# Kernel optimization log

Measured on AMD Instinct MI355X. Metric: run time of the kernel, lower is better.

The kernel has to match this reference:

```python
import jax, jax.numpy as jnp
import numpy as np


def _segment_softmax(x, seg, num_segments):
    # x: (E, C), seg: (E,) int. Numerically stable per-segment softmax along dim 0.
    m = jax.ops.segment_max(x, seg, num_segments=num_segments)  # (S, C)
    # Guard empty segments (-inf) so gather stays finite for used rows.
    e = jnp.exp(x - m[seg])                                     # (E, C)
    s = jax.ops.segment_sum(e, seg, num_segments=num_segments)  # (S, C)
    return e / s[seg]


def setup_inputs() -> dict:
    key = jax.random.key(0)
    k1, k2, k3, k4 = jax.random.split(key, 4)
    E, C, S = 16777216, 2, 4096
    return {
        "xab": jax.random.normal(k1, (E, C), dtype=jnp.float32),
        "xba": jax.random.normal(k2, (E, C), dtype=jnp.float32),
        "src_id": jax.random.randint(k3, (E,), 0, S, dtype=jnp.int64),
        "tar_id": jax.random.randint(k4, (E,), 0, S, dtype=jnp.int64),
        "num_segments": S,
    }


def reference(xab, xba, src_id, tar_id, num_segments):
    zab = _segment_softmax(xab, src_id, num_segments)  # softmax over src groups
    zba = _segment_softmax(xba, tar_id, num_segments)  # softmax over tar groups
    return (zab * zba, zab, zba)
```

## Files before the change

kernel.cpp:

```cpp
#include <hip/hip_runtime.h>

#define NSEG 4096
#define QSCALE 131072.0f
#define QINV   (1.0f / 131072.0f)

typedef unsigned long long u64;
typedef unsigned int u32;
typedef float f32x4 __attribute__((ext_vector_type(4)));
typedef float f32x2 __attribute__((ext_vector_type(2)));

__global__ __launch_bounds__(1024) void dsp_reduce_x(
    const f32x4* __restrict__ xab4, const f32x4* __restrict__ xba4,
    const int2* __restrict__ src2, const int2* __restrict__ tar2,
    float* __restrict__ partials,
    int rounds, int rs)
{
    __shared__ u64 ls[2 * NSEG];
    for (int i = threadIdx.x; i < 2 * NSEG; i += 1024) ls[i] = 0ull;
    __syncthreads();

    const int base = blockIdx.x * 1024 + threadIdx.x;
    int u = base + (rounds - 1) * rs;

    f32x4 a = xab4[u], b = xba4[u];
    int2 s = src2[u], t = tar2[u];

    for (int r = rounds - 1; r >= 0; --r) {
        int un = u - rs;
        f32x4 an, bn; int2 sn, tn;
        if (r > 0) { an = xab4[un]; bn = xba4[un]; sn = src2[un]; tn = tar2[un]; }

        u32 a0 = __float2uint_rn(__expf(a.x) * QSCALE);
        u32 a1 = __float2uint_rn(__expf(a.y) * QSCALE);
        u32 a2 = __float2uint_rn(__expf(a.z) * QSCALE);
        u32 a3 = __float2uint_rn(__expf(a.w) * QSCALE);
        atomicAdd(&ls[s.x], (u64)a0 | ((u64)a1 << 32));
        atomicAdd(&ls[s.y], (u64)a2 | ((u64)a3 << 32));

        u32 b0 = __float2uint_rn(__expf(b.x) * QSCALE);
        u32 b1 = __float2uint_rn(__expf(b.y) * QSCALE);
        u32 b2 = __float2uint_rn(__expf(b.z) * QSCALE);
        u32 b3 = __float2uint_rn(__expf(b.w) * QSCALE);
        atomicAdd(&ls[NSEG + t.x], (u64)b0 | ((u64)b1 << 32));
        atomicAdd(&ls[NSEG + t.y], (u64)b2 | ((u64)b3 << 32));

        u = un; a = an; b = bn; s = sn; t = tn;
    }
    __syncthreads();

    f32x2* dst = (f32x2*)(partials + (size_t)blockIdx.x * (4 * NSEG));
    for (int i = threadIdx.x; i < 2 * NSEG; i += 1024) {
        u64 v = ls[i];
        f32x2 w = { (float)(u32)v * QINV, (float)(u32)(v >> 32) * QINV };
        __builtin_nontemporal_store(w, &dst[i]);
    }
}

__global__ __launch_bounds__(1024) void dsp_reduce_g(
    const f32x4* __restrict__ xab4, const f32x4* __restrict__ xba4,
    const int2* __restrict__ src2, const int2* __restrict__ tar2,
    float* __restrict__ partials, int Eh)
{
    __shared__ u64 ls[2 * NSEG];
    for (int i = threadIdx.x; i < 2 * NSEG; i += 1024) ls[i] = 0ull;
    __syncthreads();

    const int stride = gridDim.x * 1024;
    for (int u = blockIdx.x * 1024 + threadIdx.x; u < Eh; u += stride) {
        f32x4 a = xab4[u]; f32x4 b = xba4[u];
        int2 s = src2[u]; int2 t = tar2[u];
        u32 a0 = __float2uint_rn(__expf(a.x) * QSCALE);
        u32 a1 = __float2uint_rn(__expf(a.y) * QSCALE);
        u32 a2 = __float2uint_rn(__expf(a.z) * QSCALE);
        u32 a3 = __float2uint_rn(__expf(a.w) * QSCALE);
        atomicAdd(&ls[s.x], (u64)a0 | ((u64)a1 << 32));
        atomicAdd(&ls[s.y], (u64)a2 | ((u64)a3 << 32));
        u32 b0 = __float2uint_rn(__expf(b.x) * QSCALE);
        u32 b1 = __float2uint_rn(__expf(b.y) * QSCALE);
        u32 b2 = __float2uint_rn(__expf(b.z) * QSCALE);
        u32 b3 = __float2uint_rn(__expf(b.w) * QSCALE);
        atomicAdd(&ls[NSEG + t.x], (u64)b0 | ((u64)b1 << 32));
        atomicAdd(&ls[NSEG + t.y], (u64)b2 | ((u64)b3 << 32));
    }
    __syncthreads();

    f32x2* dst = (f32x2*)(partials + (size_t)blockIdx.x * (4 * NSEG));
    for (int i = threadIdx.x; i < 2 * NSEG; i += 1024) {
        u64 v = ls[i];
        f32x2 w = { (float)(u32)v * QINV, (float)(u32)(v >> 32) * QINV };
        __builtin_nontemporal_store(w, &dst[i]);
    }
}

__global__ __launch_bounds__(256) void dsp_sum(
    const f32x4* __restrict__ partials, f32x4* __restrict__ rcp_out, int nb)
{
    int i = blockIdx.x * blockDim.x + threadIdx.x;
    f32x4 acc = {0.f, 0.f, 0.f, 0.f};
    for (int p = 0; p < nb; ++p) {
        f32x4 v = __builtin_nontemporal_load(&partials[(size_t)p * NSEG + i]);
        acc += v;
    }
    f32x4 r;
    r.x = (acc.x > 0.f) ? 1.f / acc.x : 0.f;
    r.y = (acc.y > 0.f) ? 1.f / acc.y : 0.f;
    r.z = (acc.z > 0.f) ? 1.f / acc.z : 0.f;
    r.w = (acc.w > 0.f) ? 1.f / acc.w : 0.f;
    rcp_out[i] = r;
}

__global__ __launch_bounds__(1024) void dsp_norm_x(
    const f32x4* __restrict__ xab4, const f32x4* __restrict__ xba4,
    const int2* __restrict__ src2, const int2* __restrict__ tar2,
    const f32x4* __restrict__ rcp_tab,
    f32x4* __restrict__ out, int rounds, int rs, int Eh)
{
    __shared__ float ls[4 * NSEG];
    for (int i = threadIdx.x; i < NSEG; i += 1024)
        ((f32x4*)ls)[i] = rcp_tab[i];
    __syncthreads();

    const int base = blockIdx.x * 1024 + threadIdx.x;
    int u = base;

    f32x4 a = xab4[u], b = xba4[u];
    int2 s = src2[u], t = tar2[u];

    for (int r = 0; r < rounds; ++r) {
        int un = u + rs;
        f32x4 an, bn; int2 sn, tn;
        if (r + 1 < rounds) { an = xab4[un]; bn = xba4[un]; sn = src2[un]; tn = tar2[un]; }

        f32x2 ra0 = *(const f32x2*)&ls[2 * s.x];
        f32x2 ra1 = *(const f32x2*)&ls[2 * s.y];
        f32x2 rb0 = *(const f32x2*)&ls[2 * NSEG + 2 * t.x];
        f32x2 rb1 = *(const f32x2*)&ls[2 * NSEG + 2 * t.y];

        f32x4 zab = { __expf(a.x) * ra0.x, __expf(a.y) * ra0.y,
                      __expf(a.z) * ra1.x, __expf(a.w) * ra1.y };
        f32x4 zba = { __expf(b.x) * rb0.x, __expf(b.y) * rb0.y,
                      __expf(b.z) * rb1.x, __expf(b.w) * rb1.y };
        f32x4 prod = zab * zba;

        __builtin_nontemporal_store(prod, &out[u]);
        __builtin_nontemporal_store(zab,  &out[Eh + u]);
        __builtin_nontemporal_store(zba,  &out[2 * Eh + u]);

        u = un; a = an; b = bn; s = sn; t = tn;
    }
}

__global__ __launch_bounds__(1024) void dsp_norm_g(
    const f32x4* __restrict__ xab4, const f32x4* __restrict__ xba4,
    const int2* __restrict__ src2, const int2* __restrict__ tar2,
    const f32x4* __restrict__ rcp_tab,
    f32x4* __restrict__ out, int Eh)
{
    __shared__ float ls[4 * NSEG];
    for (int i = threadIdx.x; i < NSEG; i += 1024)
        ((f32x4*)ls)[i] = rcp_tab[i];
    __syncthreads();

    const int stride = gridDim.x * 1024;
    for (int u = blockIdx.x * 1024 + threadIdx.x; u < Eh; u += stride) {
        f32x4 a = xab4[u]; f32x4 b = xba4[u];
        int2 s = src2[u]; int2 t = tar2[u];
        f32x2 ra0 = *(const f32x2*)&ls[2 * s.x];
        f32x2 ra1 = *(const f32x2*)&ls[2 * s.y];
        f32x2 rb0 = *(const f32x2*)&ls[2 * NSEG + 2 * t.x];
        f32x2 rb1 = *(const f32x2*)&ls[2 * NSEG + 2 * t.y];
        f32x4 zab = { __expf(a.x) * ra0.x, __expf(a.y) * ra0.y,
                      __expf(a.z) * ra1.x, __expf(a.w) * ra1.y };
        f32x4 zba = { __expf(b.x) * rb0.x, __expf(b.y) * rb0.y,
                      __expf(b.z) * rb1.x, __expf(b.w) * rb1.y };
        f32x4 prod = zab * zba;
        __builtin_nontemporal_store(prod, &out[u]);
        __builtin_nontemporal_store(zab,  &out[Eh + u]);
        __builtin_nontemporal_store(zba,  &out[2 * Eh + u]);
    }
}

extern "C" void kernel_launch(void* const* d_in, const int* in_sizes, int n_in,
                              void* d_out, int out_size, void* d_ws, size_t ws_size,
                              hipStream_t stream)
{
    const int E  = in_sizes[0] / 2;
    const int Eh = E / 2;
    const f32x4* xab4 = (const f32x4*)d_in[0];
    const f32x4* xba4 = (const f32x4*)d_in[1];
    const int2*  src2 = (const int2*)d_in[2];
    const int2*  tar2 = (const int2*)d_in[3];

    const int NB = 512;
    const int RS = NB * 1024;
    float* rcp_tab  = (float*)d_ws;
    float* partials = (float*)((char*)d_ws + 65536);
    size_t need = 65536 + (size_t)NB * 65536;
    const bool exact = (ws_size >= need) && (Eh % RS == 0) && (Eh / RS >= 1);

    if (exact) {
        const int rounds = Eh / RS;
        dsp_reduce_x<<<NB, 1024, 0, stream>>>(xab4, xba4, src2, tar2,
                                              partials, rounds, RS);
        dsp_sum<<<NSEG / 256, 256, 0, stream>>>((const f32x4*)partials,
                                                (f32x4*)rcp_tab, NB);
        dsp_norm_x<<<NB, 1024, 0, stream>>>(xab4, xba4, src2, tar2,
                                            (const f32x4*)rcp_tab,
                                            (f32x4*)d_out, rounds, RS, Eh);
    } else {
        dsp_reduce_g<<<NB, 1024, 0, stream>>>(xab4, xba4, src2, tar2,
                                              partials, Eh);
        dsp_sum<<<NSEG / 256, 256, 0, stream>>>((const f32x4*)partials,
                                                (f32x4*)rcp_tab, NB);
        dsp_norm_g<<<NB, 1024, 0, stream>>>(xab4, xba4, src2, tar2,
                                            (const f32x4*)rcp_tab,
                                            (f32x4*)d_out, Eh);
    }
}
```

Measured before the change: 429.1 us.

## Fuse reduce, sum and normalize into one cooperative kernel with grid syncs

Replaces the three-launch pipeline with a single cooperative kernel that accumulates per-block segment sums, grid-syncs, reduces partials across blocks with warp shuffles, grid-syncs again, and then normalizes. The normalize pass walks rounds in reverse so the most recently read data may still be in cache, and the partials stores become normal instead of nontemporal so they stay cached for the cross-block sum. This removes launch gaps and gives some L2/MALL reuse, at the cost of grid-sync overhead and losing the explicit software prefetch in the loops. It depends on occupancy of at least 2 blocks per CU so that all 512 blocks are co-resident.

```diff
diff --git a/kernel.cpp b/kernel.cpp
--- a/kernel.cpp
+++ b/kernel.cpp
@@ -1,34 +1,40 @@
 #include <hip/hip_runtime.h>
+#include <hip/hip_cooperative_groups.h>
+
+namespace cg = cooperative_groups;
 
 #define NSEG 4096
 #define QSCALE 131072.0f
 #define QINV   (1.0f / 131072.0f)
+#define NB 512
 
 typedef unsigned long long u64;
 typedef unsigned int u32;
 typedef float f32x4 __attribute__((ext_vector_type(4)));
 typedef float f32x2 __attribute__((ext_vector_type(2)));
 
-__global__ __launch_bounds__(1024) void dsp_reduce_x(
+__global__ __launch_bounds__(1024, 8) void dsp_fused(
     const f32x4* __restrict__ xab4, const f32x4* __restrict__ xba4,
     const int2* __restrict__ src2, const int2* __restrict__ tar2,
     float* __restrict__ partials,
-    int rounds, int rs)
+    float* __restrict__ rcp_tab,
+    f32x4* __restrict__ out,
+    int rounds, int rs, int Eh)
 {
     __shared__ u64 ls[2 * NSEG];
-    for (int i = threadIdx.x; i < 2 * NSEG; i += 1024) ls[i] = 0ull;
-    __syncthreads();
-
-    const int base = blockIdx.x * 1024 + threadIdx.x;
-    int u = base + (rounds - 1) * rs;
-
-    f32x4 a = xab4[u], b = xba4[u];
-    int2 s = src2[u], t = tar2[u];
-
-    for (int r = rounds - 1; r >= 0; --r) {
-        int un = u - rs;
-        f32x4 an, bn; int2 sn, tn;
-        if (r > 0) { an = xab4[un]; bn = xba4[un]; sn = src2[un]; tn = tar2[un]; }
+    const int tid = threadIdx.x;
+    const int bid = blockIdx.x;
+    const int base = bid * 1024 + tid;
+
+    for (int i = tid; i < 2 * NSEG; i += 1024) ls[i] = 0ull;
+    __syncthreads();
+
+    for (int r = 0; r < rounds; ++r) {
+        int u = base + r * rs;
+        f32x4 a = xab4[u];
+        f32x4 b = xba4[u];
+        int2 s = src2[u];
+        int2 t = tar2[u];
 
         u32 a0 = __float2uint_rn(__expf(a.x) * QSCALE);
         u32 a1 = __float2uint_rn(__expf(a.y) * QSCALE);
@@ -43,16 +49,61 @@
         u32 b3 = __float2uint_rn(__expf(b.w) * QSCALE);
         atomicAdd(&ls[NSEG + t.x], (u64)b0 | ((u64)b1 << 32));
         atomicAdd(&ls[NSEG + t.y], (u64)b2 | ((u64)b3 << 32));
-
-        u = un; a = an; b = bn; s = sn; t = tn;
-    }
-    __syncthreads();
-
-    f32x2* dst = (f32x2*)(partials + (size_t)blockIdx.x * (4 * NSEG));
-    for (int i = threadIdx.x; i < 2 * NSEG; i += 1024) {
-        u64 v = ls[i];
-        f32x2 w = { (float)(u32)v * QINV, (float)(u32)(v >> 32) * QINV };
-        __builtin_nontemporal_store(w, &dst[i]);
+    }
+    __syncthreads();
+
+    {
+        f32x2* dst = (f32x2*)(partials + (size_t)bid * (4 * NSEG));
+        for (int i = tid; i < 2 * NSEG; i += 1024) {
+            u64 v = ls[i];
+            f32x2 w = { (float)(u32)v * QINV, (float)(u32)(v >> 32) * QINV };
+            dst[i] = w;
+        }
+    }
+    __threadfence();
+    cg::this_grid().sync();
+
+    {
+        int cl = tid >> 5;
+        int k  = tid & 31;
+        int col = bid * 32 + cl;
+        float acc = 0.f;
+        for (int p = k; p < NB; p += 32)
+            acc += partials[(size_t)p * (4 * NSEG) + col];
+        for (int off = 16; off; off >>= 1)
+            acc += __shfl_down(acc, off, 32);
+        if (k == 0)
+            rcp_tab[col] = (acc > 0.f) ? 1.f / acc : 0.f;
+    }
+    __threadfence();
+    cg::this_grid().sync();
+
+    float* lf = (float*)ls;
+    for (int i = tid; i < NSEG; i += 1024)
+        ((f32x4*)lf)[i] = ((const f32x4*)rcp_tab)[i];
+    __syncthreads();
+
+    for (int r = rounds - 1; r >= 0; --r) {
+        int u = base + r * rs;
+        f32x4 a = xab4[u];
+        f32x4 b = xba4[u];
+        int2 s = src2[u];
+        int2 t = tar2[u];
+
+        f32x2 ra0 = *(const f32x2*)&lf[2 * s.x];
+        f32x2 ra1 = *(const f32x2*)&lf[2 * s.y];
+        f32x2 rb0 = *(const f32x2*)&lf[2 * NSEG + 2 * t.x];
+        f32x2 rb1 = *(const f32x2*)&lf[2 * NSEG + 2 * t.y];
+
+        f32x4 zab = { __expf(a.x) * ra0.x, __expf(a.y) * ra0.y,
+                      __expf(a.z) * ra1.x, __expf(a.w) * ra1.y };
+        f32x4 zba = { __expf(b.x) * rb0.x, __expf(b.y) * rb0.y,
+                      __expf(b.z) * rb1.x, __expf(b.w) * rb1.y };
+        f32x4 prod = zab * zba;
+
+        __builtin_nontemporal_store(prod, &out[u]);
+        __builtin_nontemporal_store(zab,  &out[Eh + u]);
+        __builtin_nontemporal_store(zba,  &out[2 * Eh + u]);
     }
 }
 
@@ -88,7 +139,7 @@
     for (int i = threadIdx.x; i < 2 * NSEG; i += 1024) {
         u64 v = ls[i];
         f32x2 w = { (float)(u32)v * QINV, (float)(u32)(v >> 32) * QINV };
-        __builtin_nontemporal_store(w, &dst[i]);
+        dst[i] = w;
     }
 }
 
@@ -97,57 +148,14 @@
 {
     int i = blockIdx.x * blockDim.x + threadIdx.x;
     f32x4 acc = {0.f, 0.f, 0.f, 0.f};
-    for (int p = 0; p < nb; ++p) {
-        f32x4 v = __builtin_nontemporal_load(&partials[(size_t)p * NSEG + i]);
-        acc += v;
-    }
+    for (int p = 0; p < nb; ++p)
+        acc += partials[(size_t)p * NSEG + i];
     f32x4 r;
     r.x = (acc.x > 0.f) ? 1.f / acc.x : 0.f;
     r.y = (acc.y > 0.f) ? 1.f / acc.y : 0.f;
     r.z = (acc.z > 0.f) ? 1.f / acc.z : 0.f;
     r.w = (acc.w > 0.f) ? 1.f / acc.w : 0.f;
     rcp_out[i] = r;
-}
-
-__global__ __launch_bounds__(1024) void dsp_norm_x(
-    const f32x4* __restrict__ xab4, const f32x4* __restrict__ xba4,
-    const int2* __restrict__ src2, const int2* __restrict__ tar2,
-    const f32x4* __restrict__ rcp_tab,
-    f32x4* __restrict__ out, int rounds, int rs, int Eh)
-{
-    __shared__ float ls[4 * NSEG];
-    for (int i = threadIdx.x; i < NSEG; i += 1024)
-        ((f32x4*)ls)[i] = rcp_tab[i];
-    __syncthreads();
-
-    const int base = blockIdx.x * 1024 + threadIdx.x;
-    int u = base;
-
-    f32x4 a = xab4[u], b = xba4[u];
-    int2 s = src2[u], t = tar2[u];
-
-    for (int r = 0; r < rounds; ++r) {
-        int un = u + rs;
-        f32x4 an, bn; int2 sn, tn;
-        if (r + 1 < rounds) { an = xab4[un]; bn = xba4[un]; sn = src2[un]; tn = tar2[un]; }
-
-        f32x2 ra0 = *(const f32x2*)&ls[2 * s.x];
-        f32x2 ra1 = *(const f32x2*)&ls[2 * s.y];
-        f32x2 rb0 = *(const f32x2*)&ls[2 * NSEG + 2 * t.x];
-        f32x2 rb1 = *(const f32x2*)&ls[2 * NSEG + 2 * t.y];
-
-        f32x4 zab = { __expf(a.x) * ra0.x, __expf(a.y) * ra0.y,
-                      __expf(a.z) * ra1.x, __expf(a.w) * ra1.y };
-        f32x4 zba = { __expf(b.x) * rb0.x, __expf(b.y) * rb0.y,
-                      __expf(b.z) * rb1.x, __expf(b.w) * rb1.y };
-        f32x4 prod = zab * zba;
-
-        __builtin_nontemporal_store(prod, &out[u]);
-        __builtin_nontemporal_store(zab,  &out[Eh + u]);
-        __builtin_nontemporal_store(zba,  &out[2 * Eh + u]);
-
-        u = un; a = an; b = bn; s = sn; t = tn;
-    }
 }
 
 __global__ __launch_bounds__(1024) void dsp_norm_g(
@@ -191,22 +199,26 @@
     const int2*  src2 = (const int2*)d_in[2];
     const int2*  tar2 = (const int2*)d_in[3];
 
-    const int NB = 512;
     const int RS = NB * 1024;
     float* rcp_tab  = (float*)d_ws;
     float* partials = (float*)((char*)d_ws + 65536);
     size_t need = 65536 + (size_t)NB * 65536;
-    const bool exact = (ws_size >= need) && (Eh % RS == 0) && (Eh / RS >= 1);
-
-    if (exact) {
-        const int rounds = Eh / RS;
-        dsp_reduce_x<<<NB, 1024, 0, stream>>>(xab4, xba4, src2, tar2,
-                                              partials, rounds, RS);
-        dsp_sum<<<NSEG / 256, 256, 0, stream>>>((const f32x4*)partials,
-                                                (f32x4*)rcp_tab, NB);
-        dsp_norm_x<<<NB, 1024, 0, stream>>>(xab4, xba4, src2, tar2,
-                                            (const f32x4*)rcp_tab,
-                                            (f32x4*)d_out, rounds, RS, Eh);
+
+    int rounds = Eh / RS;
+    bool exact = (ws_size >= need) && (Eh % RS == 0) && (rounds >= 1);
+
+    int occ = 0;
+    (void)hipOccupancyMaxActiveBlocksPerMultiprocessor(&occ, dsp_fused, 1024, 0);
+
+    if (exact && occ >= 2) {
+        f32x4* outv = (f32x4*)d_out;
+        void* args[] = { (void*)&xab4, (void*)&xba4, (void*)&src2, (void*)&tar2,
+                         (void*)&partials, (void*)&rcp_tab, (void*)&outv,
+                         (void*)&rounds, (void*)&(int&)RS, (void*)&(int&)Eh };
+        int rs_v = RS, eh_v = Eh;
+        args[7] = (void*)&rounds; args[8] = (void*)&rs_v; args[9] = (void*)&eh_v;
+        (void)hipLaunchCooperativeKernel((void*)dsp_fused, dim3(NB), dim3(1024),
+                                         args, 0, stream);
     } else {
         dsp_reduce_g<<<NB, 1024, 0, stream>>>(xab4, xba4, src2, tar2,
                                               partials, Eh);
```

Result: faster. 356.9 us (-16.8%).

## Batch loads four-deep in reduce, prefetch two rounds in normalize, drop nontemporal hints

Applied to the files above, without the earlier changes.

The reduction kernel now uses 512-thread blocks with an occupancy hint and issues four independent load groups per iteration before its LDS atomics, instead of a one-deep software prefetch. The normalize kernel prefetches two rounds ahead rather than one and declares a minimum of 8 blocks. Partials are now written and read with regular loads and stores instead of nontemporal ones, so they can stay in cache for the sum kernel. The fallback path is now gated on workspace size. The aim is more memory-level parallelism to hide load latency, at the cost of higher register pressure.

```diff
diff --git a/kernel.cpp b/kernel.cpp
--- a/kernel.cpp
+++ b/kernel.cpp
@@ -3,48 +3,86 @@
 #define NSEG 4096
 #define QSCALE 131072.0f
 #define QINV   (1.0f / 131072.0f)
+#define NB 512
 
 typedef unsigned long long u64;
 typedef unsigned int u32;
 typedef float f32x4 __attribute__((ext_vector_type(4)));
 typedef float f32x2 __attribute__((ext_vector_type(2)));
 
-__global__ __launch_bounds__(1024) void dsp_reduce_x(
+__device__ __forceinline__ u64 packexp(float x, float y) {
+    u32 lo = __float2uint_rn(__expf(x) * QSCALE);
+    u32 hi = __float2uint_rn(__expf(y) * QSCALE);
+    return (u64)lo | ((u64)hi << 32);
+}
+
+__global__ __launch_bounds__(512, 4) void dsp_reduce_x(
     const f32x4* __restrict__ xab4, const f32x4* __restrict__ xba4,
     const int2* __restrict__ src2, const int2* __restrict__ tar2,
     float* __restrict__ partials,
-    int rounds, int rs)
+    int groups, int stride)
+{
+    __shared__ u64 ls[2 * NSEG];
+    for (int i = threadIdx.x; i < 2 * NSEG; i += 512) ls[i] = 0ull;
+    __syncthreads();
+
+    const int base = blockIdx.x * 512 + threadIdx.x;
+    for (int g = 0; g < groups; ++g) {
+        const int u0 = base + (4 * g) * stride;
+        const int u1 = u0 + stride, u2 = u1 + stride, u3 = u2 + stride;
+
+        f32x4 a0 = xab4[u0], a1 = xab4[u1], a2 = xab4[u2], a3 = xab4[u3];
+        f32x4 b0 = xba4[u0], b1 = xba4[u1], b2 = xba4[u2], b3 = xba4[u3];
+        int2  s0 = src2[u0], s1 = src2[u1], s2 = src2[u2], s3 = src2[u3];
+        int2  t0 = tar2[u0], t1 = tar2[u1], t2 = tar2[u2], t3 = tar2[u3];
+
+        atomicAdd(&ls[s0.x], packexp(a0.x, a0.y));
+        atomicAdd(&ls[s0.y], packexp(a0.z, a0.w));
+        atomicAdd(&ls[NSEG + t0.x], packexp(b0.x, b0.y));
+        atomicAdd(&ls[NSEG + t0.y], packexp(b0.z, b0.w));
+
+        atomicAdd(&ls[s1.x], packexp(a1.x, a1.y));
+        atomicAdd(&ls[s1.y], packexp(a1.z, a1.w));
+        atomicAdd(&ls[NSEG + t1.x], packexp(b1.x, b1.y));
+        atomicAdd(&ls[NSEG + t1.y], packexp(b1.z, b1.w));
+
+        atomicAdd(&ls[s2.x], packexp(a2.x, a2.y));
+        atomicAdd(&ls[s2.y], packexp(a2.z, a2.w));
+        atomicAdd(&ls[NSEG + t2.x], packexp(b2.x, b2.y));
+        atomicAdd(&ls[NSEG + t2.y], packexp(b2.z, b2.w));
+
+        atomicAdd(&ls[s3.x], packexp(a3.x, a3.y));
+        atomicAdd(&ls[s3.y], packexp(a3.z, a3.w));
+        atomicAdd(&ls[NSEG + t3.x], packexp(b3.x, b3.y));
+        atomicAdd(&ls[NSEG + t3.y], packexp(b3.z, b3.w));
+    }
+    __syncthreads();
+
+    f32x2* dst = (f32x2*)(partials + (size_t)blockIdx.x * (4 * NSEG));
+    for (int i = threadIdx.x; i < 2 * NSEG; i += 512) {
+        u64 v = ls[i];
+        f32x2 w = { (float)(u32)v * QINV, (float)(u32)(v >> 32) * QINV };
+        dst[i] = w;
+    }
+}
+
+__global__ __launch_bounds__(1024) void dsp_reduce_g(
+    const f32x4* __restrict__ xab4, const f32x4* __restrict__ xba4,
+    const int2* __restrict__ src2, const int2* __restrict__ tar2,
+    float* __restrict__ partials, int Eh)
 {
     __shared__ u64 ls[2 * NSEG];
     for (int i = threadIdx.x; i < 2 * NSEG; i += 1024) ls[i] = 0ull;
     __syncthreads();
 
-    const int base = blockIdx.x * 1024 + threadIdx.x;
-    int u = base + (rounds - 1) * rs;
-
-    f32x4 a = xab4[u], b = xba4[u];
-    int2 s = src2[u], t = tar2[u];
-
-    for (int r = rounds - 1; r >= 0; --r) {
-        int un = u - rs;
-        f32x4 an, bn; int2 sn, tn;
-        if (r > 0) { an = xab4[un]; bn = xba4[un]; sn = src2[un]; tn = tar2[un]; }
-
-        u32 a0 = __float2uint_rn(__expf(a.x) * QSCALE);
-        u32 a1 = __float2uint_rn(__expf(a.y) * QSCALE);
-        u32 a2 = __float2uint_rn(__expf(a.z) * QSCALE);
-        u32 a3 = __float2uint_rn(__expf(a.w) * QSCALE);
-        atomicAdd(&ls[s.x], (u64)a0 | ((u64)a1 << 32));
-        atomicAdd(&ls[s.y], (u64)a2 | ((u64)a3 << 32));
-
-        u32 b0 = __float2uint_rn(__expf(b.x) * QSCALE);
-        u32 b1 = __float2uint_rn(__expf(b.y) * QSCALE);
-        u32 b2 = __float2uint_rn(__expf(b.z) * QSCALE);
-        u32 b3 = __float2uint_rn(__expf(b.w) * QSCALE);
-        atomicAdd(&ls[NSEG + t.x], (u64)b0 | ((u64)b1 << 32));
-        atomicAdd(&ls[NSEG + t.y], (u64)b2 | ((u64)b3 << 32));
-
-        u = un; a = an; b = bn; s = sn; t = tn;
+    const int stride = gridDim.x * 1024;
+    for (int u = blockIdx.x * 1024 + threadIdx.x; u < Eh; u += stride) {
+        f32x4 a = xab4[u]; f32x4 b = xba4[u];
+        int2 s = src2[u]; int2 t = tar2[u];
+        atomicAdd(&ls[s.x], packexp(a.x, a.y));
+        atomicAdd(&ls[s.y], packexp(a.z, a.w));
+        atomicAdd(&ls[NSEG + t.x], packexp(b.x, b.y));
+        atomicAdd(&ls[NSEG + t.y], packexp(b.z, b.w));
     }
     __syncthreads();
 
@@ -52,43 +90,7 @@
     for (int i = threadIdx.x; i < 2 * NSEG; i += 1024) {
         u64 v = ls[i];
         f32x2 w = { (float)(u32)v * QINV, (float)(u32)(v >> 32) * QINV };
-        __builtin_nontemporal_store(w, &dst[i]);
-    }
-}
-
-__global__ __launch_bounds__(1024) void dsp_reduce_g(
-    const f32x4* __restrict__ xab4, const f32x4* __restrict__ xba4,
-    const int2* __restrict__ src2, const int2* __restrict__ tar2,
-    float* __restrict__ partials, int Eh)
-{
-    __shared__ u64 ls[2 * NSEG];
-    for (int i = threadIdx.x; i < 2 * NSEG; i += 1024) ls[i] = 0ull;
-    __syncthreads();
-
-    const int stride = gridDim.x * 1024;
-    for (int u = blockIdx.x * 1024 + threadIdx.x; u < Eh; u += stride) {
-        f32x4 a = xab4[u]; f32x4 b = xba4[u];
-        int2 s = src2[u]; int2 t = tar2[u];
-        u32 a0 = __float2uint_rn(__expf(a.x) * QSCALE);
-        u32 a1 = __float2uint_rn(__expf(a.y) * QSCALE);
-        u32 a2 = __float2uint_rn(__expf(a.z) * QSCALE);
-        u32 a3 = __float2uint_rn(__expf(a.w) * QSCALE);
-        atomicAdd(&ls[s.x], (u64)a0 | ((u64)a1 << 32));
-        atomicAdd(&ls[s.y], (u64)a2 | ((u64)a3 << 32));
-        u32 b0 = __float2uint_rn(__expf(b.x) * QSCALE);
-        u32 b1 = __float2uint_rn(__expf(b.y) * QSCALE);
-        u32 b2 = __float2uint_rn(__expf(b.z) * QSCALE);
-        u32 b3 = __float2uint_rn(__expf(b.w) * QSCALE);
-        atomicAdd(&ls[NSEG + t.x], (u64)b0 | ((u64)b1 << 32));
-        atomicAdd(&ls[NSEG + t.y], (u64)b2 | ((u64)b3 << 32));
-    }
-    __syncthreads();
-
-    f32x2* dst = (f32x2*)(partials + (size_t)blockIdx.x * (4 * NSEG));
-    for (int i = threadIdx.x; i < 2 * NSEG; i += 1024) {
-        u64 v = ls[i];
-        f32x2 w = { (float)(u32)v * QINV, (float)(u32)(v >> 32) * QINV };
-        __builtin_nontemporal_store(w, &dst[i]);
+        dst[i] = w;
     }
 }
 
@@ -97,10 +99,8 @@
 {
     int i = blockIdx.x * blockDim.x + threadIdx.x;
     f32x4 acc = {0.f, 0.f, 0.f, 0.f};
-    for (int p = 0; p < nb; ++p) {
-        f32x4 v = __builtin_nontemporal_load(&partials[(size_t)p * NSEG + i]);
-        acc += v;
-    }
+    for (int p = 0; p < nb; ++p)
+        acc += partials[(size_t)p * NSEG + i];
     f32x4 r;
     r.x = (acc.x > 0.f) ? 1.f / acc.x : 0.f;
     r.y = (acc.y > 0.f) ? 1.f / acc.y : 0.f;
@@ -109,7 +109,7 @@
     rcp_out[i] = r;
 }
 
-__global__ __launch_bounds__(1024) void dsp_norm_x(
+__global__ __launch_bounds__(1024, 8) void dsp_norm_x(
     const f32x4* __restrict__ xab4, const f32x4* __restrict__ xba4,
     const int2* __restrict__ src2, const int2* __restrict__ tar2,
     const f32x4* __restrict__ rcp_tab,
@@ -121,32 +121,38 @@
     __syncthreads();
 
     const int base = blockIdx.x * 1024 + threadIdx.x;
-    int u = base;
-
-    f32x4 a = xab4[u], b = xba4[u];
-    int2 s = src2[u], t = tar2[u];
+
+    f32x4 a0 = xab4[base], b0 = xba4[base];
+    int2  s0 = src2[base], t0 = tar2[base];
+    f32x4 a1, b1; int2 s1, t1;
+    if (rounds > 1) {
+        int u1 = base + rs;
+        a1 = xab4[u1]; b1 = xba4[u1]; s1 = src2[u1]; t1 = tar2[u1];
+    }
 
     for (int r = 0; r < rounds; ++r) {
-        int un = u + rs;
+        int u = base + r * rs;
+        int up = u + 2 * rs;
         f32x4 an, bn; int2 sn, tn;
-        if (r + 1 < rounds) { an = xab4[un]; bn = xba4[un]; sn = src2[un]; tn = tar2[un]; }
-
-        f32x2 ra0 = *(const f32x2*)&ls[2 * s.x];
-        f32x2 ra1 = *(const f32x2*)&ls[2 * s.y];
-        f32x2 rb0 = *(const f32x2*)&ls[2 * NSEG + 2 * t.x];
-        f32x2 rb1 = *(const f32x2*)&ls[2 * NSEG + 2 * t.y];
-
-        f32x4 zab = { __expf(a.x) * ra0.x, __expf(a.y) * ra0.y,
-                      __expf(a.z) * ra1.x, __expf(a.w) * ra1.y };
-        f32x4 zba = { __expf(b.x) * rb0.x, __expf(b.y) * rb0.y,
-                      __expf(b.z) * rb1.x, __expf(b.w) * rb1.y };
+        if (r + 2 < rounds) { an = xab4[up]; bn = xba4[up]; sn = src2[up]; tn = tar2[up]; }
+
+        f32x2 ra0 = *(const f32x2*)&ls[2 * s0.x];
+        f32x2 ra1 = *(const f32x2*)&ls[2 * s0.y];
+        f32x2 rb0 = *(const f32x2*)&ls[2 * NSEG + 2 * t0.x];
+        f32x2 rb1 = *(const f32x2*)&ls[2 * NSEG + 2 * t0.y];
+
+        f32x4 zab = { __expf(a0.x) * ra0.x, __expf(a0.y) * ra0.y,
+                      __expf(a0.z) * ra1.x, __expf(a0.w) * ra1.y };
+        f32x4 zba = { __expf(b0.x) * rb0.x, __expf(b0.y) * rb0.y,
+                      __expf(b0.z) * rb1.x, __expf(b0.w) * rb1.y };
         f32x4 prod = zab * zba;
 
         __builtin_nontemporal_store(prod, &out[u]);
         __builtin_nontemporal_store(zab,  &out[Eh + u]);
         __builtin_nontemporal_store(zba,  &out[2 * Eh + u]);
 
-        u = un; a = an; b = bn; s = sn; t = tn;
+        a0 = a1; b0 = b1; s0 = s1; t0 = t1;
+        a1 = an; b1 = bn; s1 = sn; t1 = tn;
     }
 }
 
@@ -191,23 +197,26 @@
     const int2*  src2 = (const int2*)d_in[2];
     const int2*  tar2 = (const int2*)d_in[3];
 
-    const int NB = 512;
-    const int RS = NB * 1024;
     float* rcp_tab  = (float*)d_ws;
     float* partials = (float*)((char*)d_ws + 65536);
     size_t need = 65536 + (size_t)NB * 65536;
-    const bool exact = (ws_size >= need) && (Eh % RS == 0) && (Eh / RS >= 1);
+
+    const int RSTRIDE = NB * 512;
+    const int NSPAN   = NB * 1024;
+    bool exact = (ws_size >= need) &&
+                 (Eh % (4 * RSTRIDE) == 0) && (Eh % NSPAN == 0);
 
     if (exact) {
-        const int rounds = Eh / RS;
-        dsp_reduce_x<<<NB, 1024, 0, stream>>>(xab4, xba4, src2, tar2,
-                                              partials, rounds, RS);
+        int groups = Eh / (4 * RSTRIDE);
+        int rounds = Eh / NSPAN;
+        dsp_reduce_x<<<NB, 512, 0, stream>>>(xab4, xba4, src2, tar2,
+                                             partials, groups, RSTRIDE);
         dsp_sum<<<NSEG / 256, 256, 0, stream>>>((const f32x4*)partials,
                                                 (f32x4*)rcp_tab, NB);
         dsp_norm_x<<<NB, 1024, 0, stream>>>(xab4, xba4, src2, tar2,
                                             (const f32x4*)rcp_tab,
-                                            (f32x4*)d_out, rounds, RS, Eh);
-    } else {
+                                            (f32x4*)d_out, rounds, NSPAN, Eh);
+    } else if (ws_size >= need) {
         dsp_reduce_g<<<NB, 1024, 0, stream>>>(xab4, xba4, src2, tar2,
                                               partials, Eh);
         dsp_sum<<<NSEG / 256, 256, 0, stream>>>((const f32x4*)partials,
```

Result: faster. 378.4 us (-11.8%).
